# Kernel optimization log

Hardware: AMD Instinct MI355X
Metric: run time of the kernel (lower is better)

## Reference

```python
import jax, jax.numpy as jnp
import numpy as np
import math

HIDDEN = 2048
HEADS = 16
G = 4          # kv groups (= self.num_group after the module's head_num//num_group)
HPG = HEADS // G  # q heads per group
D = HIDDEN // HEADS  # 128


def setup_inputs() -> dict:
    key = jax.random.key(0)
    ks = jax.random.split(key, 9)
    B, S = 2, 2048
    s = 0.02
    return {
        "x": jax.random.normal(ks[0], (B, S, HIDDEN), dtype=jnp.float32),
        "Wq": jax.random.normal(ks[1], (HIDDEN, HIDDEN), dtype=jnp.float32) * s,
        "bq": jnp.zeros((HIDDEN,), jnp.float32),
        "Wk": jax.random.normal(ks[2], (HIDDEN, G * D), dtype=jnp.float32) * s,
        "bk": jnp.zeros((G * D,), jnp.float32),
        "Wv": jax.random.normal(ks[3], (HIDDEN, G * D), dtype=jnp.float32) * s,
        "bv": jnp.zeros((G * D,), jnp.float32),
        "Wo": jax.random.normal(ks[4], (HIDDEN, HIDDEN), dtype=jnp.float32) * s,
        "bo": jnpp if False else jnp.zeros((HIDDEN,), jnp.float32),
    }


def reference(x, Wq, bq, Wk, bk, Wv, bv, Wo, bo):
    B, S, H = x.shape
    # projections (torch Linear with W stored as (in, out))
    q = (x @ Wq + bq).reshape(B, S, G, HPG, D)   # (B,S,G,Hpg,D)
    k = (x @ Wk + bk).reshape(B, S, G, D)        # (B,S,G,D)
    v = (x @ Wv + bv).reshape(B, S, G, D)
    scale = 1.0 / math.sqrt(D)
    # scores: each of the Hpg query heads in a group shares the group's K/V
    scores = jnp.einsum("bsghd,btgd->bghst", q, k) * scale  # (B,G,Hpg,S,S)
    attn = jax.nn.softmax(scores, axis=-1)
    # dropout is identity in eval mode
    o = jnp.einsum("bghst,btgd->bsghd", attn, v).reshape(B, S, H)
    return o @ Wo + bo
```

## Files before the change

### kernel.cpp

```cpp
#include <hip/hip_runtime.h>

#define HID   2048
#define KD    2048
#define GQ    4
#define HPGQ  4
#define DH    128
#define SEQ   2048
#define NBATCH 2
#define NTOK  (NBATCH * SEQ)
#define NQKV  3072

typedef unsigned short u16;
typedef unsigned int   u32;
using bf16x8 = __attribute__((ext_vector_type(8))) __bf16;
using bf16x2 = __attribute__((ext_vector_type(2))) __bf16;
using f32x4  = __attribute__((ext_vector_type(4))) float;
using u32x4  = __attribute__((ext_vector_type(4))) u32;

#if __has_builtin(__builtin_amdgcn_exp2f)
#define FEXP2(x) __builtin_amdgcn_exp2f(x)
#else
#define FEXP2(x) exp2f(x)
#endif

#define QSCALE 0.12751744f

__device__ __forceinline__ u16 f2bf(float f) {
  union { float f; u32 u; } v; v.f = f;
  u32 u = v.u + 0x7fffu + ((v.u >> 16) & 1u);
  return (u16)(u >> 16);
}

__device__ __forceinline__ u32 pk2(float a, float b) {
  bf16x2 t;
  t[0] = (__bf16)a;
  t[1] = (__bf16)b;
  return __builtin_bit_cast(u32, t);
}

__device__ __forceinline__ void gl16(const void* g, void* l) {
  __builtin_amdgcn_global_load_lds((const __attribute__((address_space(1))) u32*)g,
                                   (__attribute__((address_space(3))) u32*)l, 16, 0, 0);
}

__device__ __forceinline__ int swz(int r, int c) {
  return (c & ~7) | ((c ^ r ^ (r >> 3)) & 7);
}

__global__ __launch_bounds__(256) void k_cvt_bf16(const float* __restrict__ in,
                                                  u16* __restrict__ out, int n4) {
  int i = blockIdx.x * 256 + threadIdx.x;
  if (i < n4) {
    const float4 v = ((const float4*)in)[i];
    ushort4 o;
    o.x = f2bf(v.x); o.y = f2bf(v.y); o.z = f2bf(v.z); o.w = f2bf(v.w);
    ((ushort4*)out)[i] = o;
  }
}

__global__ __launch_bounds__(256) void k_trans_cvt(const float* __restrict__ W,
                                                   u16* __restrict__ WT,
                                                   int K, int N, int rowoff) {
  __shared__ float tile[32][33];
  const int tx = threadIdx.x, ty = threadIdx.y;
  const int k0 = blockIdx.y * 32, n0 = blockIdx.x * 32;
#pragma unroll
  for (int i = 0; i < 4; ++i)
    tile[ty + 8 * i][tx] = W[(size_t)(k0 + ty + 8 * i) * N + (n0 + tx)];
  __syncthreads();
#pragma unroll
  for (int i = 0; i < 4; ++i)
    WT[(size_t)(rowoff + n0 + ty + 8 * i) * K + (k0 + tx)] = f2bf(tile[tx][ty + 8 * i]);
}


#define GEMM_STEP(CUR, NXT, K0N, PRE)                                              \
  do {                                                                             \
    if (PRE) {                                                                     \
      const u16* aB = A  + (size_t)m0 * KD + (K0N);                                \
      const u16* bB = Bt + (size_t)n0 * KD + (K0N);                                \
      _Pragma("unroll")                                                            \
      for (int i = 0; i < 2; ++i) {                                                \
        gl16(aB + stOff[i], S + (NXT)*4096 + (i * 256 + t) * 8);                   \
        gl16(bB + stOff[i], S + 8192 + (NXT)*4096 + (i * 256 + t) * 8);            \
      }                                                                            \
      asm volatile("s_waitcnt vmcnt(4)" ::: "memory");                             \
    } else {                                                                       \
      asm volatile("s_waitcnt vmcnt(0)" ::: "memory");                             \
    }                                                                              \
    __builtin_amdgcn_s_barrier();                                                  \
    bf16x8 af[4], bfr[4];                                                          \
    _Pragma("unroll")                                                              \
    for (int m = 0; m < 4; ++m)                                                    \
      af[m] = *(const bf16x8*)((const char*)S + (CUR)*8192 + m * 1024 + aAddr);    \
    _Pragma("unroll")                                                              \
    for (int n = 0; n < 4; ++n)                                                    \
      bfr[n] = *(const bf16x8*)((const char*)S + 16384 + (CUR)*8192 + n * 1024 + bAddr); \
    __builtin_amdgcn_s_setprio(1);                                                 \
    _Pragma("unroll")                                                              \
    for (int m = 0; m < 4; ++m)                                                    \
      _Pragma("unroll")                                                            \
      for (int n = 0; n < 4; ++n)                                                  \
        acc[m][n] = __builtin_amdgcn_mfma_f32_16x16x32_bf16(af[m], bfr[n], acc[m][n], 0, 0, 0); \
    __builtin_amdgcn_s_setprio(0);                                                 \
    __builtin_amdgcn_s_barrier();                                                  \
  } while (0)

#define GEMM_PROLOG()                                                              \
  __shared__ u16 S[16384];                                                         \
  const int t = threadIdx.x, l = t & 63, w = t >> 6;                               \
  const int lr = l & 15, lk = l >> 4;                                              \
  const int wr = w >> 1, wc = w & 1;                                               \
  const int m0 = blockIdx.y * 128, n0 = blockIdx.x * 128;                          \
  int stOff[2];                                                                    \
  _Pragma("unroll")                                                                \
  for (int i = 0; i < 2; ++i) {                                                    \
    const int e = i * 256 + t;                                                     \
    const int r = e >> 2;                                                          \
    const int cs = (e & 3) ^ ((r >> 1) & 3);                                       \
    stOff[i] = r * KD + cs * 8;                                                    \
  }                                                                                \
  const int axor = (lk ^ ((lr >> 1) & 3)) << 4;                                    \
  const int aAddr = (wr * 64 + lr) * 64 + axor;                                    \
  const int bAddr = (wc * 64 + lr) * 64 + axor;                                    \
  f32x4 acc[4][4] = {};                                                            \
  {                                                                                \
    const u16* aB = A  + (size_t)m0 * KD;                                          \
    const u16* bB = Bt + (size_t)n0 * KD;                                          \
    _Pragma("unroll")                                                              \
    for (int i = 0; i < 2; ++i) {                                                  \
      gl16(aB + stOff[i], S + (i * 256 + t) * 8);                                  \
      gl16(bB + stOff[i], S + 8192 + (i * 256 + t) * 8);                           \
    }                                                                              \
  }                                                                                \
  for (int kt = 0; kt < KD / 32 - 2; kt += 2) {                                    \
    GEMM_STEP(0, 1, (kt + 1) * 32, true);                                          \
    GEMM_STEP(1, 0, (kt + 2) * 32, true);                                          \
  }                                                                                \
  GEMM_STEP(0, 1, (KD / 32 - 1) * 32, true);                                       \
  GEMM_STEP(1, 0, 0, false);

__global__ __launch_bounds__(256) void k_gemm_qkv(
    const u16* __restrict__ A, const u16* __restrict__ Bt,
    u16* __restrict__ qkv, u16* __restrict__ vT,
    const float* __restrict__ bq, const float* __restrict__ bk,
    const float* __restrict__ bv) {
  GEMM_PROLOG()

  const int gm = m0 + wr * 64, gn = n0 + wc * 64;
#pragma unroll
  for (int m = 0; m < 4; ++m) {
    const int row0 = gm + m * 16 + lk * 4;
#pragma unroll
    for (int n = 0; n < 4; ++n) {
      const int col = gn + n * 16 + lr;
      float bias, qs = 1.0f;
      if (col < HID) { bias = bq[col]; qs = QSCALE; }
      else if (col < HID + 512) bias = bk[col - HID];
      else bias = bv[col - HID - 512];
      if (col < HID + 512) {
#pragma unroll
        for (int r = 0; r < 4; ++r)
          qkv[(size_t)(row0 + r) * NQKV + col] = f2bf((acc[m][n][r] + bias) * qs);
      } else {
        const int gg = (col - 2560) >> 7, d = (col - 2560) & 127;
        const int b = row0 >> 11, s0 = row0 & 2047;
        ushort4 pk;
        pk.x = f2bf(acc[m][n][0] + bias);
        pk.y = f2bf(acc[m][n][1] + bias);
        pk.z = f2bf(acc[m][n][2] + bias);
        pk.w = f2bf(acc[m][n][3] + bias);
        *(ushort4*)(vT + ((size_t)(b * GQ + gg) * DH + d) * SEQ + s0) = pk;
      }
    }
  }
}

__global__ __launch_bounds__(256) void k_gemm_o(
    const u16* __restrict__ A, const u16* __restrict__ Bt,
    const float* __restrict__ bo, float* __restrict__ C) {
  GEMM_PROLOG()

  const int gm = m0 + wr * 64, gn = n0 + wc * 64;
#pragma unroll
  for (int m = 0; m < 4; ++m) {
    const int row0 = gm + m * 16 + lk * 4;
#pragma unroll
    for (int n = 0; n < 4; ++n) {
      const int col = gn + n * 16 + lr;
      const float bias = bo[col];
#pragma unroll
      for (int r = 0; r < 4; ++r)
        C[(size_t)(row0 + r) * HID + col] = acc[m][n][r] + bias;
    }
  }
}


#define ATTN_ITER(KS, VS, KN, VN, TTV, PRE)                                        \
  do {                                                                             \
    if (PRE) {                                                                     \
      const int t0n = ((start + (TTV) + 1) & (NT - 1)) * 32;                       \
      const u16* kbT = kbase + (size_t)t0n * NQKV;                                 \
      const u16* vbT = vbase + t0n;                                                \
      _Pragma("unroll")                                                            \
      for (int i = 0; i < 2; ++i) {                                                \
        gl16(kbT + kOffE[i], (KN) + (i * 256 + t) * 8);                            \
        gl16(vbT + vOffE[i], (VN) + (i * 256 + t) * 8);                            \
      }                                                                            \
      asm volatile("s_waitcnt vmcnt(4)" ::: "memory");                             \
    } else {                                                                       \
      asm volatile("s_waitcnt vmcnt(0)" ::: "memory");                             \
    }                                                                              \
    __builtin_amdgcn_s_barrier();                                                  \
    f32x4 sc[2][2] = {};                                                           \
    __builtin_amdgcn_s_setprio(1);                                                 \
    _Pragma("unroll")                                                              \
    for (int kk = 0; kk < 4; ++kk) {                                               \
      bf16x8 kf[2];                                                                \
      _Pragma("unroll")                                                            \
      for (int mk = 0; mk < 2; ++mk) {                                             \
        const int LIT = (mk << 12) ^ ((kk >> 1) << 7) ^ ((kk & 1) << 6) ^ (mk << 5); \
        kf[mk] = *(const bf16x8*)((const char*)(KS) + (kQ0 ^ LIT));                \
      }                                                                            \
      _Pragma("unroll")                                                            \
      for (int nq = 0; nq < 2; ++nq)                                               \
        _Pragma("unroll")                                                          \
        for (int mk = 0; mk < 2; ++mk)                                             \
          sc[nq][mk] = __builtin_amdgcn_mfma_f32_16x16x32_bf16(kf[mk], qf[nq][kk], sc[nq][mk], 0, 0, 0); \
    }                                                                              \
    __builtin_amdgcn_s_setprio(0);                                                 \
    bf16x8 pa[2];                                                                  \
    _Pragma("unroll")                                                              \
    for (int nq = 0; nq < 2; ++nq) {                                               \
      u32 w0 = pk2(FEXP2(sc[nq][0][0]), FEXP2(sc[nq][0][1]));                      \
      u32 w1 = pk2(FEXP2(sc[nq][0][2]), FEXP2(sc[nq][0][3]));                      \
      u32 w2 = pk2(FEXP2(sc[nq][1][0]), FEXP2(sc[nq][1][1]));                      \
      u32 w3 = pk2(FEXP2(sc[nq][1][2]), FEXP2(sc[nq][1][3]));                      \
      asm("v_permlane32_swap_b32 %0, %1" : "+v"(w0), "+v"(w2));                    \
      asm("v_permlane32_swap_b32 %0, %1" : "+v"(w1), "+v"(w3));                    \
      asm("v_permlane16_swap_b32 %0, %1" : "+v"(w0), "+v"(w2));                    \
      asm("v_permlane16_swap_b32 %0, %1" : "+v"(w1), "+v"(w3));                    \
      u32x4 u = {w0, w1, w2, w3};                                                  \
      pa[nq] = __builtin_bit_cast(bf16x8, u);                                      \
    }                                                                              \
    __builtin_amdgcn_s_setprio(1);                                                 \
    _Pragma("unroll")                                                              \
    for (int nq = 0; nq < 2; ++nq)                                                 \
      acc_s[nq] = __builtin_amdgcn_mfma_f32_16x16x32_bf16(pa[nq], vones, acc_s[nq], 0, 0, 0); \
    _Pragma("unroll")                                                              \
    for (int nd = 0; nd < 8; ++nd) {                                               \
      const bf16x8 vf = *(const bf16x8*)((const char*)(VS) + vQ0 + nd * 1024);     \
      _Pragma("unroll")                                                            \
      for (int nq = 0; nq < 2; ++nq)                                               \
        acc_o[nq][nd] = __builtin_amdgcn_mfma_f32_16x16x32_bf16(pa[nq], vf, acc_o[nq][nd], 0, 0, 0); \
    }                                                                              \
    __builtin_amdgcn_s_setprio(0);                                                 \
    __builtin_amdgcn_s_barrier();                                                  \
  } while (0)

__global__ __launch_bounds__(256, 2) void k_attn(
    const u16* __restrict__ qkv, const u16* __restrict__ vT, u16* __restrict__ o_ws) {
  __shared__ u16 smem[16384];
  u16* const kb0 = smem;
  u16* const kb1 = smem + 4096;
  u16* const vb0 = smem + 8192;
  u16* const vb1 = smem + 12288;

  const int t = threadIdx.x, l = t & 63, w = t >> 6;
  const int lr = l & 15, lk = l >> 4;
  const int f = blockIdx.x;
  const int bg = f & 7;
  const int h = (f >> 3) & 3;
  const int qt = f >> 5;
  const int b = bg >> 2, g = bg & 3;
  const int q0 = qt * 128;
  const int qcol = (g * HPGQ + h) * DH;
  const u16* qbase = qkv + (size_t)(b * SEQ) * NQKV;
  const u16* kbase = qbase + HID + g * DH;
  const u16* vbase = vT + (size_t)(b * GQ + g) * DH * SEQ;

  const int NT = SEQ / 32;
  const int start = (qt * 5 + h * 9) & (NT - 1);

  const int kQ0 = lr * 256 + ((lk ^ (lr & 7) ^ (lr >> 3)) << 4);
  const int vQ0 = lr * 64 + ((lk ^ ((lr >> 1) & 3)) << 4);
  int kOffE[2], vOffE[2];
#pragma unroll
  for (int i = 0; i < 2; ++i) {
    const int e = i * 256 + t;
    const int r = e >> 4, c = e & 15;
    kOffE[i] = r * NQKV + swz(r, c) * 8;
    const int rv = e >> 2, cv = e & 3;
    vOffE[i] = rv * SEQ + ((cv ^ ((rv >> 1) & 3)) * 8);
  }

  bf16x8 qf[2][4];
#pragma unroll
  for (int nq = 0; nq < 2; ++nq)
#pragma unroll
    for (int kk = 0; kk < 4; ++kk)
      qf[nq][kk] = *(const bf16x8*)(qbase + (size_t)(q0 + w * 32 + nq * 16 + lr) * NQKV +
                                    qcol + kk * 32 + lk * 8);

  {
    const int t00 = start * 32;
    const u16* kbT = kbase + (size_t)t00 * NQKV;
    const u16* vbT = vbase + t00;
#pragma unroll
    for (int i = 0; i < 2; ++i) {
      gl16(kbT + kOffE[i], kb0 + (i * 256 + t) * 8);
      gl16(vbT + vOffE[i], vb0 + (i * 256 + t) * 8);
    }
  }

  f32x4 acc_o[2][8] = {};
  f32x4 acc_s[2] = {};

  bf16x8 vones;
#pragma unroll
  for (int j = 0; j < 8; ++j) vones[j] = (lr == 0) ? (__bf16)1.0f : (__bf16)0.0f;

  for (int tp = 0; tp < NT - 2; tp += 2) {
    ATTN_ITER(kb0, vb0, kb1, vb1, tp, true);
    ATTN_ITER(kb1, vb1, kb0, vb0, tp + 1, true);
  }
  ATTN_ITER(kb0, vb0, kb1, vb1, NT - 2, true);
  ATTN_ITER(kb1, vb1, kb0, vb0, NT - 1, false);

#pragma unroll
  for (int nq = 0; nq < 2; ++nq)
#pragma unroll
    for (int r = 0; r < 4; ++r) {
      const float s = __shfl(acc_s[nq][r], l & 48);
      const float inv = 1.0f / s;
      const int q = q0 + w * 32 + nq * 16 + lk * 4 + r;
#pragma unroll
      for (int nd = 0; nd < 8; ++nd) {
        const int d = nd * 16 + lr;
        o_ws[(size_t)(b * SEQ + q) * HID + qcol + d] = f2bf(acc_o[nq][nd][r] * inv);
      }
    }
}

extern "C" void kernel_launch(void* const* d_in, const int* in_sizes, int n_in,
                              void* d_out, int out_size, void* d_ws, size_t ws_size,
                              hipStream_t stream) {
  const float* x  = (const float*)d_in[0];
  const float* Wq = (const float*)d_in[1];
  const float* bq = (const float*)d_in[2];
  const float* Wk = (const float*)d_in[3];
  const float* bk = (const float*)d_in[4];
  const float* Wv = (const float*)d_in[5];
  const float* bv = (const float*)d_in[6];
  const float* Wo = (const float*)d_in[7];
  const float* bo = (const float*)d_in[8];
  float* out = (float*)d_out;

  char* ws = (char*)d_ws;
  u16* x_bf  = (u16*)ws;  ws += (size_t)NTOK * KD * 2;
  u16* qkvT  = (u16*)ws;  ws += (size_t)NQKV * KD * 2;
  u16* WoT   = (u16*)ws;  ws += (size_t)HID * KD * 2;
  u16* qkv   = (u16*)ws;  ws += (size_t)NTOK * NQKV * 2;
  u16* vTb   = (u16*)ws;  ws += (size_t)NBATCH * GQ * DH * SEQ * 2;
  u16* o_ws  = x_bf;

  k_cvt_bf16<<<(NTOK * KD / 4 + 255) / 256, 256, 0, stream>>>(x, x_bf, NTOK * KD / 4);
  k_trans_cvt<<<dim3(HID / 32, KD / 32), dim3(32, 8), 0, stream>>>(Wq, qkvT, KD, HID, 0);
  k_trans_cvt<<<dim3(512 / 32, KD / 32), dim3(32, 8), 0, stream>>>(Wk, qkvT, KD, 512, 2048);
  k_trans_cvt<<<dim3(512 / 32, KD / 32), dim3(32, 8), 0, stream>>>(Wv, qkvT, KD, 512, 2560);
  k_trans_cvt<<<dim3(HID / 32, KD / 32), dim3(32, 8), 0, stream>>>(Wo, WoT, KD, HID, 0);

  k_gemm_qkv<<<dim3(NQKV / 128, NTOK / 128), 256, 0, stream>>>(x_bf, qkvT, qkv, vTb, bq, bk, bv);
  k_attn<<<SEQ / 128 * NBATCH * GQ * HPGQ, 256, 0, stream>>>(qkv, vTb, o_ws);
  k_gemm_o<<<dim3(HID / 128, NTOK / 128), 256, 0, stream>>>(o_ws, WoT, bo, out);
}
```

Baseline: 211.9 us.

## Rewrite QKV GEMM with 256x256 tiles, 8 waves, and quadrant-interleaved LDS pipeline

```diff
diff --git a/kernel.cpp b/kernel.cpp
--- a/kernel.cpp
+++ b/kernel.cpp
@@ -74,86 +74,113 @@
 }
 
 
-#define GEMM_STEP(CUR, NXT, K0N, PRE)                                              \
+#define STG256(OP, ROWB, KTB, LB)                                                  \
+  { _Pragma("unroll") for (int i = 0; i < 2; ++i)                                  \
+      gl16((OP) + (size_t)(ROWB) * KD + (KTB) + stOffE[i],                         \
+           S + (LB) + (i * 512 + t) * 8); }
+
+#define STAGE_TILE(D, KTB)                                                         \
+  STG256(A,  m0,       (KTB), (D) * 32768 + 0);                                    \
+  STG256(A,  m0 + 128, (KTB), (D) * 32768 + 8192);                                 \
+  STG256(Bt, n0,       (KTB), (D) * 32768 + 16384);                                \
+  STG256(Bt, n0 + 128, (KTB), (D) * 32768 + 24576);
+
+#define RDA(D, M, KC) (*(const bf16x8*)((const char*)S + (D) * 65536 + (M) * 2048 + (aQ ^ ((KC) << 6))))
+#define RDB(D, N, KC) (*(const bf16x8*)((const char*)S + (D) * 65536 + (N) * 2048 + (bQ ^ ((KC) << 6))))
+
+#define MFMA16(MB, NB)                                                             \
+  __builtin_amdgcn_s_setprio(1);                                                   \
+  _Pragma("unroll") for (int m = 0; m < 4; ++m)                                    \
+    _Pragma("unroll") for (int n = 0; n < 2; ++n)                                  \
+      _Pragma("unroll") for (int kc = 0; kc < 2; ++kc)                             \
+        acc[(MB) + m][(NB) + n] = __builtin_amdgcn_mfma_f32_16x16x32_bf16(         \
+            afr[m][kc], bfr[(NB) + n][kc], acc[(MB) + m][(NB) + n], 0, 0, 0);      \
+  __builtin_amdgcn_s_setprio(0);
+
+#define ITER256(D, KTN, PRE)                                                       \
   do {                                                                             \
+                                     \
+    _Pragma("unroll") for (int m = 0; m < 4; ++m)                                  \
+      _Pragma("unroll") for (int kc = 0; kc < 2; ++kc)                             \
+        afr[m][kc] = RDA(D, m, kc);                                                \
+    _Pragma("unroll") for (int n = 0; n < 2; ++n)                                  \
+      _Pragma("unroll") for (int kc = 0; kc < 2; ++kc)                             \
+        bfr[n][kc] = RDB(D, n, kc);                                                \
+    __builtin_amdgcn_s_barrier();                                                  \
+    MFMA16(0, 0)                                                                   \
+    __builtin_amdgcn_s_barrier();                                                  \
+                                             \
+    _Pragma("unroll") for (int n = 2; n < 4; ++n)                                  \
+      _Pragma("unroll") for (int kc = 0; kc < 2; ++kc)                             \
+        bfr[n][kc] = RDB(D, n, kc);                                                \
+    __builtin_amdgcn_s_barrier();                                                  \
+    MFMA16(0, 2)                                                                   \
+    __builtin_amdgcn_s_barrier();                                                  \
+                                 \
+    _Pragma("unroll") for (int m = 0; m < 4; ++m)                                  \
+      _Pragma("unroll") for (int kc = 0; kc < 2; ++kc)                             \
+        afr[m][kc] = RDA(D, 4 + m, kc);                                            \
+    __builtin_amdgcn_s_barrier();                                                  \
+    MFMA16(4, 2)                                                                   \
+    __builtin_amdgcn_s_barrier();                                                  \
+             \
     if (PRE) {                                                                     \
-      const u16* aB = A  + (size_t)m0 * KD + (K0N);                                \
-      const u16* bB = Bt + (size_t)n0 * KD + (K0N);                                \
-      _Pragma("unroll")                                                            \
-      for (int i = 0; i < 2; ++i) {                                                \
-        gl16(aB + stOff[i], S + (NXT)*4096 + (i * 256 + t) * 8);                   \
-        gl16(bB + stOff[i], S + 8192 + (NXT)*4096 + (i * 256 + t) * 8);            \
-      }                                                                            \
-      asm volatile("s_waitcnt vmcnt(4)" ::: "memory");                             \
+      STAGE_TILE(D, KTN);                                                          \
+      asm volatile("s_waitcnt vmcnt(8)" ::: "memory");                             \
     } else {                                                                       \
       asm volatile("s_waitcnt vmcnt(0)" ::: "memory");                             \
     }                                                                              \
     __builtin_amdgcn_s_barrier();                                                  \
-    bf16x8 af[4], bfr[4];                                                          \
-    _Pragma("unroll")                                                              \
-    for (int m = 0; m < 4; ++m)                                                    \
-      af[m] = *(const bf16x8*)((const char*)S + (CUR)*8192 + m * 1024 + aAddr);    \
-    _Pragma("unroll")                                                              \
-    for (int n = 0; n < 4; ++n)                                                    \
-      bfr[n] = *(const bf16x8*)((const char*)S + 16384 + (CUR)*8192 + n * 1024 + bAddr); \
-    __builtin_amdgcn_s_setprio(1);                                                 \
-    _Pragma("unroll")                                                              \
-    for (int m = 0; m < 4; ++m)                                                    \
-      _Pragma("unroll")                                                            \
-      for (int n = 0; n < 4; ++n)                                                  \
-        acc[m][n] = __builtin_amdgcn_mfma_f32_16x16x32_bf16(af[m], bfr[n], acc[m][n], 0, 0, 0); \
-    __builtin_amdgcn_s_setprio(0);                                                 \
+    MFMA16(4, 0)                                                                   \
     __builtin_amdgcn_s_barrier();                                                  \
   } while (0)
 
-#define GEMM_PROLOG()                                                              \
-  __shared__ u16 S[16384];                                                         \
-  const int t = threadIdx.x, l = t & 63, w = t >> 6;                               \
-  const int lr = l & 15, lk = l >> 4;                                              \
-  const int wr = w >> 1, wc = w & 1;                                               \
-  const int m0 = blockIdx.y * 128, n0 = blockIdx.x * 128;                          \
-  int stOff[2];                                                                    \
-  _Pragma("unroll")                                                                \
-  for (int i = 0; i < 2; ++i) {                                                    \
-    const int e = i * 256 + t;                                                     \
-    const int r = e >> 2;                                                          \
-    const int cs = (e & 3) ^ ((r >> 1) & 3);                                       \
-    stOff[i] = r * KD + cs * 8;                                                    \
-  }                                                                                \
-  const int axor = (lk ^ ((lr >> 1) & 3)) << 4;                                    \
-  const int aAddr = (wr * 64 + lr) * 64 + axor;                                    \
-  const int bAddr = (wc * 64 + lr) * 64 + axor;                                    \
-  f32x4 acc[4][4] = {};                                                            \
-  {                                                                                \
-    const u16* aB = A  + (size_t)m0 * KD;                                          \
-    const u16* bB = Bt + (size_t)n0 * KD;                                          \
-    _Pragma("unroll")                                                              \
-    for (int i = 0; i < 2; ++i) {                                                  \
-      gl16(aB + stOff[i], S + (i * 256 + t) * 8);                                  \
-      gl16(bB + stOff[i], S + 8192 + (i * 256 + t) * 8);                           \
-    }                                                                              \
-  }                                                                                \
-  for (int kt = 0; kt < KD / 32 - 2; kt += 2) {                                    \
-    GEMM_STEP(0, 1, (kt + 1) * 32, true);                                          \
-    GEMM_STEP(1, 0, (kt + 2) * 32, true);                                          \
-  }                                                                                \
-  GEMM_STEP(0, 1, (KD / 32 - 1) * 32, true);                                       \
-  GEMM_STEP(1, 0, 0, false);
-
-__global__ __launch_bounds__(256) void k_gemm_qkv(
+__global__ __launch_bounds__(512, 1) void k_gemm_qkv(
     const u16* __restrict__ A, const u16* __restrict__ Bt,
     u16* __restrict__ qkv, u16* __restrict__ vT,
     const float* __restrict__ bq, const float* __restrict__ bk,
     const float* __restrict__ bv) {
-  GEMM_PROLOG()
-
-  const int gm = m0 + wr * 64, gn = n0 + wc * 64;
-#pragma unroll
-  for (int m = 0; m < 4; ++m) {
-    const int row0 = gm + m * 16 + lk * 4;
+  __shared__ u16 S[65536];
+  const int t = threadIdx.x, l = t & 63, w = t >> 6;
+  const int lr = l & 15, lk = l >> 4;
+  const int wm = w >> 2, wn = w & 3;
+  const int m0 = blockIdx.y * 256, n0 = blockIdx.x * 256;
+
+  int stOffE[2];
+#pragma unroll
+  for (int i = 0; i < 2; ++i) {
+    const int e = i * 512 + t;
+    const int r = e >> 3;
+    stOffE[i] = r * KD + ((e & 7) ^ (r & 7)) * 8;
+  }
+  const int qb = lr * 128 + (((lr >> 2) & 1) << 6) + ((lk ^ (lr & 3)) << 4);
+  const int aQ = wm * 16384 + qb;
+  const int bQ = 32768 + (wn >> 1) * 16384 + (wn & 1) * 8192 + qb;
+
+  f32x4 acc[8][4] = {};
+  bf16x8 afr[4][2], bfr[4][2];
+
+  STAGE_TILE(0, 0);
+  STAGE_TILE(1, 64);
+  asm volatile("s_waitcnt vmcnt(8)" ::: "memory");
+  __builtin_amdgcn_s_barrier();
+
+  for (int j = 0; j < 28; j += 2) {
+    ITER256(0, (j + 2) * 64, true);
+    ITER256(1, (j + 3) * 64, true);
+  }
+  ITER256(0, 30 * 64, true);
+  ITER256(1, 31 * 64, true);
+  ITER256(0, 0, false);
+  ITER256(1, 0, false);
+
+  const int gmB = m0 + wm * 128, gnB = n0 + wn * 64;
+#pragma unroll
+  for (int m = 0; m < 8; ++m) {
+    const int row0 = gmB + m * 16 + lk * 4;
 #pragma unroll
     for (int n = 0; n < 4; ++n) {
-      const int col = gn + n * 16 + lr;
+      const int col = gnB + n * 16 + lr;
       float bias, qs = 1.0f;
       if (col < HID) { bias = bq[col]; qs = QSCALE; }
       else if (col < HID + 512) bias = bk[col - HID];
@@ -176,10 +203,73 @@
   }
 }
 
+#define GEMM_STEP(CUR, NXT, K0N, PRE)                                              \
+  do {                                                                             \
+    if (PRE) {                                                                     \
+      const u16* aB = A  + (size_t)m0 * KD + (K0N);                                \
+      const u16* bB = Bt + (size_t)n0 * KD + (K0N);                                \
+      _Pragma("unroll")                                                            \
+      for (int i = 0; i < 2; ++i) {                                                \
+        gl16(aB + stOff[i], S + (NXT)*4096 + (i * 256 + t) * 8);                   \
+        gl16(bB + stOff[i], S + 8192 + (NXT)*4096 + (i * 256 + t) * 8);            \
+      }                                                                            \
+      asm volatile("s_waitcnt vmcnt(4)" ::: "memory");                             \
+    } else {                                                                       \
+      asm volatile("s_waitcnt vmcnt(0)" ::: "memory");                             \
+    }                                                                              \
+    __builtin_amdgcn_s_barrier();                                                  \
+    bf16x8 af[4], bfr[4];                                                          \
+    _Pragma("unroll")                                                              \
+    for (int m = 0; m < 4; ++m)                                                    \
+      af[m] = *(const bf16x8*)((const char*)S + (CUR)*8192 + m * 1024 + aAddr);    \
+    _Pragma("unroll")                                                              \
+    for (int n = 0; n < 4; ++n)                                                    \
+      bfr[n] = *(const bf16x8*)((const char*)S + 16384 + (CUR)*8192 + n * 1024 + bAddr); \
+    __builtin_amdgcn_s_setprio(1);                                                 \
+    _Pragma("unroll")                                                              \
+    for (int m = 0; m < 4; ++m)                                                    \
+      _Pragma("unroll")                                                            \
+      for (int n = 0; n < 4; ++n)                                                  \
+        acc[m][n] = __builtin_amdgcn_mfma_f32_16x16x32_bf16(af[m], bfr[n], acc[m][n], 0, 0, 0); \
+    __builtin_amdgcn_s_setprio(0);                                                 \
+    __builtin_amdgcn_s_barrier();                                                  \
+  } while (0)
+
 __global__ __launch_bounds__(256) void k_gemm_o(
     const u16* __restrict__ A, const u16* __restrict__ Bt,
     const float* __restrict__ bo, float* __restrict__ C) {
-  GEMM_PROLOG()
+  __shared__ u16 S[16384];
+  const int t = threadIdx.x, l = t & 63, w = t >> 6;
+  const int lr = l & 15, lk = l >> 4;
+  const int wr = w >> 1, wc = w & 1;
+  const int m0 = blockIdx.y * 128, n0 = blockIdx.x * 128;
+  int stOff[2];
+#pragma unroll
+  for (int i = 0; i < 2; ++i) {
+    const int e = i * 256 + t;
+    const int r = e >> 2;
+    const int cs = (e & 3) ^ ((r >> 1) & 3);
+    stOff[i] = r * KD + cs * 8;
+  }
+  const int axor = (lk ^ ((lr >> 1) & 3)) << 4;
+  const int aAddr = (wr * 64 + lr) * 64 + axor;
+  const int bAddr = (wc * 64 + lr) * 64 + axor;
+  f32x4 acc[4][4] = {};
+  {
+    const u16* aB = A  + (size_t)m0 * KD;
+    const u16* bB = Bt + (size_t)n0 * KD;
+#pragma unroll
+    for (int i = 0; i < 2; ++i) {
+      gl16(aB + stOff[i], S + (i * 256 + t) * 8);
+      gl16(bB + stOff[i], S + 8192 + (i * 256 + t) * 8);
+    }
+  }
+  for (int kt = 0; kt < KD / 32 - 2; kt += 2) {
+    GEMM_STEP(0, 1, (kt + 1) * 32, true);
+    GEMM_STEP(1, 0, (kt + 2) * 32, true);
+  }
+  GEMM_STEP(0, 1, (KD / 32 - 1) * 32, true);
+  GEMM_STEP(1, 0, 0, false);
 
   const int gm = m0 + wr * 64, gn = n0 + wc * 64;
 #pragma unroll
@@ -195,7 +285,6 @@
     }
   }
 }
-
 
 #define ATTN_ITER(KS, VS, KN, VN, TTV, PRE)                                        \
   do {                                                                             \
@@ -371,7 +460,7 @@
   k_trans_cvt<<<dim3(512 / 32, KD / 32), dim3(32, 8), 0, stream>>>(Wv, qkvT, KD, 512, 2560);
   k_trans_cvt<<<dim3(HID / 32, KD / 32), dim3(32, 8), 0, stream>>>(Wo, WoT, KD, HID, 0);
 
-  k_gemm_qkv<<<dim3(NQKV / 128, NTOK / 128), 256, 0, stream>>>(x_bf, qkvT, qkv, vTb, bq, bk, bv);
+  k_gemm_qkv<<<dim3(NQKV / 256, NTOK / 256), 512, 0, stream>>>(x_bf, qkvT, qkv, vTb, bq, bk, bv);
   k_attn<<<SEQ / 128 * NBATCH * GQ * HPGQ, 256, 0, stream>>>(qkv, vTb, o_ws);
   k_gemm_o<<<dim3(HID / 128, NTOK / 128), 256, 0, stream>>>(o_ws, WoT, bo, out);
 }
```

After: 206.5 us. 2.6% less time.
